# Kernel tuning notes

Measured on AMD Instinct MI355X. Metric: run time of the kernel, lower is better.

Reference implementation:

```python
import jax, jax.numpy as jnp
import numpy as np

N = 50000
E = 800000
IN_DIM = 128
HID = 64
OUT_DIM = 1
NEG_SLOPE = 0.2
EPS = 1e-16


def _glorot(key, shape):
    fan = shape[-1] + (shape[0] if len(shape) > 1 else shape[-1])
    lim = jnp.sqrt(6.0 / fan)
    return jax.random.uniform(key, shape, jnp.float32, -lim, lim)


def setup_inputs() -> dict:
    key = jax.random.key(0)
    ks = jax.random.split(key, 12)
    x = jax.random.normal(ks[0], (N, IN_DIM), jnp.float32)
    edge_index = jax.random.randint(ks[1], (2, E), 0, N, jnp.int64)
    # GATConv layer 1: in=128, out=64, heads=4, concat=True
    W1 = _glorot(ks[2], (4 * HID, IN_DIM))
    att_src1 = _glorot(ks[3], (4, HID))
    att_dst1 = _glorot(ks[4], (4, HID))
    b1 = jnp.zeros((4 * HID,), jnp.float32)
    # GATConv layer 2: in=256, out=64, heads=1, concat=True
    W2 = _glorot(ks[5], (HID, 4 * HID))
    att_src2 = _glorot(ks[6], (1, HID))
    att_dst2 = _glorot(ks[7], (1, HID))
    b2 = jnp.zeros((HID,), jnp.float32)
    # final Linear(hidden, 1)
    fc_w = _glorot(ks[8], (OUT_DIM, HID))
    fc_b = jnp.zeros((OUT_DIM,), jnp.float32)
    return {"x": x, "edge_index": edge_index, "W1": W1, "att_src1": att_src1,
            "att_dst1": att_dst1, "b1": b1, "W2": W2, "att_src2": att_src2,
            "att_dst2": att_dst2, "b2": b2, "fc_w": fc_w, "fc_b": fc_b}


def _gat_layer(x, src, dst, W, att_src, att_dst, bias, heads, out_ch):
    n = x.shape[0]
    xt = (x @ W.T).reshape(n, heads, out_ch)          # [N, H, C]
    a_src = jnp.sum(xt * att_src[None], axis=-1)      # [N, H]
    a_dst = jnp.sum(xt * att_dst[None], axis=-1)      # [N, H]
    e = a_src[src] + a_dst[dst]                       # [E', H]
    e = jnp.where(e > 0, e, NEG_SLOPE * e)            # LeakyReLU(0.2)
    # segment softmax over incoming edges of each dst node
    m = jax.ops.segment_max(e, dst, num_segments=n)
    e = jnp.exp(e - m[dst])
    s = jax.ops.segment_sum(e, dst, num_segments=n)
    alpha = e / (s[dst] + EPS)                        # [E', H]
    msg = xt[src] * alpha[:, :, None]                 # [E', H, C]
    out = jax.ops.segment_sum(msg, dst, num_segments=n)
    return out.reshape(n, heads * out_ch) + bias


def reference(x, edge_index, W1, att_src1, att_dst1, b1,
              W2, att_src2, att_dst2, b2, fc_w, fc_b):
    n = x.shape[0]
    # PyG GATConv default: add self-loops
    loops = jnp.arange(n, dtype=edge_index.dtype)
    src = jnp.concatenate([edge_index[0], loops])
    dst = jnp.concatenate([edge_index[1], loops])
    h = jax.nn.relu(_gat_layer(x, src, dst, W1, att_src1, att_dst1, b1, 4, HID))
    h = jax.nn.relu(_gat_layer(h, src, dst, W2, att_src2, att_dst2, b2, 1, HID))
    logits = h @ fc_w.T + fc_b                        # [N, 1]
    return jax.nn.sigmoid(logits).squeeze()
```

## Files before the change

### kernel.cpp

```cpp
#include <hip/hip_runtime.h>
#include <hip/hip_bf16.h>

#define NN 50000
#define EE 800000
#define ET (NN + EE)
#define SG ((NN + 255) / 256)

typedef __attribute__((ext_vector_type(8))) short short8;
typedef __attribute__((ext_vector_type(4))) float f32x4;

__device__ __forceinline__ float bf2f(unsigned short u) {
    union { unsigned int i; float f; } v; v.i = ((unsigned int)u) << 16; return v.f;
}
__device__ __forceinline__ unsigned short f2bf(float f) {
    __hip_bfloat16 h = __float2bfloat16(f);
    return *reinterpret_cast<unsigned short*>(&h);
}
__device__ __forceinline__ float lrelu(float e) { return e > 0.f ? e : 0.2f * e; }


__global__ void k_init_cnt(int* __restrict__ cnt) {
    int i = blockIdx.x * blockDim.x + threadIdx.x;
    if (i < NN) cnt[i] = 1;
}

__global__ void k_hist(const int* __restrict__ dst, int* __restrict__ cnt) {
    int i = blockIdx.x * blockDim.x + threadIdx.x;
    if (i < EE) atomicAdd(&cnt[dst[i]], 1);
}

__global__ __launch_bounds__(256) void k_scan1(const int* __restrict__ cnt,
                                               int* __restrict__ tmp, int* __restrict__ bsum) {
    int b = blockIdx.x, t = threadIdx.x, i = b * 256 + t;
    int lane = t & 63, w = t >> 6;
    int v = (i < NN) ? cnt[i] : 0;
    int s = v;
    #pragma unroll
    for (int off = 1; off < 64; off <<= 1) {
        int u = __shfl_up(s, off);
        if (lane >= off) s += u;
    }
    __shared__ int ws[4];
    if (lane == 63) ws[w] = s;
    __syncthreads();
    if (t == 0) {
        int a = 0;
        #pragma unroll
        for (int k = 0; k < 4; k++) { int x = ws[k]; ws[k] = a; a += x; }
        bsum[b] = a;
    }
    __syncthreads();
    s += ws[w];
    if (i < NN) tmp[i] = s;
}

__global__ __launch_bounds__(256) void k_scan2(const int* __restrict__ bsum, int* __restrict__ boff) {
    int t = threadIdx.x, lane = t & 63, w = t >> 6;
    int v = (t < SG) ? bsum[t] : 0;
    int s = v;
    #pragma unroll
    for (int off = 1; off < 64; off <<= 1) {
        int u = __shfl_up(s, off);
        if (lane >= off) s += u;
    }
    __shared__ int ws[4];
    if (lane == 63) ws[w] = s;
    __syncthreads();
    if (t == 0) {
        int a = 0;
        #pragma unroll
        for (int k = 0; k < 4; k++) { int x = ws[k]; ws[k] = a; a += x; }
    }
    __syncthreads();
    s += ws[w];
    if (t < SG) boff[t] = s - v;
}

__global__ void k_scan3_prep(const int* __restrict__ tmp, const int* __restrict__ boff,
                             int* __restrict__ rowptr, int* __restrict__ writeptr,
                             int* __restrict__ csr, int* __restrict__ dstarr) {
    int i = blockIdx.x * blockDim.x + threadIdx.x;
    if (i == 0) rowptr[0] = 0;
    if (i < NN) {
        int incl = tmp[i] + boff[i >> 8];
        rowptr[i + 1] = incl;
        int v = (i & 255) ? tmp[i - 1] + boff[i >> 8] : boff[i >> 8];
        csr[v] = i;
        dstarr[v] = i;
        writeptr[i] = v + 1;
    }
}

__global__ void k_scatter(const int* __restrict__ src, const int* __restrict__ dst,
                          int* __restrict__ writeptr, int* __restrict__ csr,
                          int* __restrict__ dstarr) {
    int i = blockIdx.x * blockDim.x + threadIdx.x;
    if (i < EE) {
        int d = dst[i];
        int pos = atomicAdd(&writeptr[d], 1);
        csr[pos] = src[i];
        dstarr[pos] = d;
    }
}

template<int K, int N, int NH, bool A_BF16>
__global__ __launch_bounds__(256) void k_gemm_mfma(
    const void* __restrict__ Aptr, const float* __restrict__ W,
    const float* __restrict__ atts, const float* __restrict__ attd,
    unsigned short* __restrict__ C, float* __restrict__ as_, float* __restrict__ ad_,
    int M)
{
    constexpr int KU  = K / 8;
    constexpr int KUH = KU / 2;
    constexpr int KC  = K / 32;
    constexpr int NW  = N / 4;
    constexpr int NI  = NW / 16;
    constexpr int ABYTES = 64 * KU * 16;
    constexpr int BBYTES = N * KUH * 16;
    constexpr int SMEM = ABYTES + BBYTES + (NH == 1 ? 2048 : 0);
    __shared__ char smem[SMEM];
    char* Ash = smem;
    char* Bsh = smem + ABYTES;
    unsigned short* Csh = (unsigned short*)smem;
    float* scsh = (float*)(smem + ABYTES + BBYTES);

    int t = threadIdx.x;
    int lane = t & 63, w = t >> 6;
    int colL = lane & 15, quad = lane >> 4;
    int m0 = blockIdx.x * 64;

    {
        constexpr int CNT = 64 * KU / 256;
        #pragma unroll
        for (int i = 0; i < CNT; i++) {
            int v = t + 256 * i;
            int m = v / KU, u = v % KU;
            int gr = m0 + m; if (gr >= M) gr = M - 1;
            short8 val;
            if (A_BF16) {
                val = *(const short8*)((const unsigned short*)Aptr + (size_t)gr * K + u * 8);
            } else {
                const float* Af = (const float*)Aptr;
                float4 lo = *(const float4*)(Af + (size_t)gr * K + u * 8);
                float4 hi = *(const float4*)(Af + (size_t)gr * K + u * 8 + 4);
                val[0] = (short)f2bf(lo.x); val[1] = (short)f2bf(lo.y);
                val[2] = (short)f2bf(lo.z); val[3] = (short)f2bf(lo.w);
                val[4] = (short)f2bf(hi.x); val[5] = (short)f2bf(hi.y);
                val[6] = (short)f2bf(hi.z); val[7] = (short)f2bf(hi.w);
            }
            *(short8*)(Ash + ((size_t)m * KU + (u ^ (m & 7))) * 16) = val;
        }
    }

    f32x4 acc[4][NI];
    #pragma unroll
    for (int mi = 0; mi < 4; mi++)
        #pragma unroll
        for (int ni = 0; ni < NI; ni++) acc[mi][ni] = (f32x4){0.f, 0.f, 0.f, 0.f};

    #pragma unroll
    for (int kh = 0; kh < 2; kh++) {
        __syncthreads();
        {
            constexpr int CNT = N * KUH / 256;
            #pragma unroll
            for (int i = 0; i < CNT; i++) {
                int v = t + 256 * i;
                int n = v / KUH, uu = v % KUH;
                int u = kh * KUH + uu;
                float4 lo = *(const float4*)(W + (size_t)n * K + u * 8);
                float4 hi = *(const float4*)(W + (size_t)n * K + u * 8 + 4);
                short8 val;
                val[0] = (short)f2bf(lo.x); val[1] = (short)f2bf(lo.y);
                val[2] = (short)f2bf(lo.z); val[3] = (short)f2bf(lo.w);
                val[4] = (short)f2bf(hi.x); val[5] = (short)f2bf(hi.y);
                val[6] = (short)f2bf(hi.z); val[7] = (short)f2bf(hi.w);
                *(short8*)(Bsh + ((size_t)n * KUH + (uu ^ (n & 7))) * 16) = val;
            }
        }
        __syncthreads();
        #pragma unroll
        for (int kcl = 0; kcl < KC / 2; kcl++) {
            int uA = (kh * (KC / 2) + kcl) * 4 + quad;
            int uB = kcl * 4 + quad;
            short8 bf[NI];
            #pragma unroll
            for (int ni = 0; ni < NI; ni++) {
                int n = w * NW + ni * 16 + colL;
                bf[ni] = *(const short8*)(Bsh + ((size_t)n * KUH + (uB ^ (n & 7))) * 16);
            }
            #pragma unroll
            for (int mi = 0; mi < 4; mi++) {
                int m = mi * 16 + colL;
                short8 af = *(const short8*)(Ash + ((size_t)m * KU + (uA ^ (m & 7))) * 16);
                #pragma unroll
                for (int ni = 0; ni < NI; ni++)
                    acc[mi][ni] = __builtin_amdgcn_mfma_f32_16x16x32_bf16(af, bf[ni], acc[mi][ni], 0, 0, 0);
            }
        }
    }
    __syncthreads();

    float asv[NI], adv[NI];
    #pragma unroll
    for (int ni = 0; ni < NI; ni++) {
        int na = (NH == 4) ? (w * 64 + ni * 16 + colL) : (w * 16 + colL);
        asv[ni] = atts[na];
        adv[ni] = attd[na];
    }
    #pragma unroll
    for (int mi = 0; mi < 4; mi++) {
        float ps[4] = {0.f, 0.f, 0.f, 0.f}, pd[4] = {0.f, 0.f, 0.f, 0.f};
        #pragma unroll
        for (int ni = 0; ni < NI; ni++)
            #pragma unroll
            for (int r = 0; r < 4; r++) {
                ps[r] += acc[mi][ni][r] * asv[ni];
                pd[r] += acc[mi][ni][r] * adv[ni];
            }
        #pragma unroll
        for (int off = 1; off < 16; off <<= 1)
            #pragma unroll
            for (int r = 0; r < 4; r++) {
                ps[r] += __shfl_xor(ps[r], off);
                pd[r] += __shfl_xor(pd[r], off);
            }
        if (colL == 0) {
            #pragma unroll
            for (int r = 0; r < 4; r++) {
                int rloc = mi * 16 + quad * 4 + r;
                if (NH == 4) {
                    int row = m0 + rloc;
                    if (row < M) {
                        as_[(size_t)row * 4 + w] = ps[r];
                        ad_[(size_t)row * 4 + w] = pd[r];
                    }
                } else {
                    scsh[(w * 64 + rloc) * 2 + 0] = ps[r];
                    scsh[(w * 64 + rloc) * 2 + 1] = pd[r];
                }
            }
        }
    }

    #pragma unroll
    for (int mi = 0; mi < 4; mi++)
        #pragma unroll
        for (int ni = 0; ni < NI; ni++)
            #pragma unroll
            for (int r = 0; r < 4; r++)
                Csh[(size_t)(mi * 16 + quad * 4 + r) * (N + 8) + w * NW + ni * 16 + colL] =
                    f2bf(acc[mi][ni][r]);
    __syncthreads();

    {
        constexpr int CNT = 64 * (N / 8) / 256;
        #pragma unroll
        for (int i = 0; i < CNT; i++) {
            int v = t + 256 * i;
            int m = v / (N / 8), u = v % (N / 8);
            int row = m0 + m;
            if (row < M)
                *(short8*)(C + (size_t)row * N + u * 8) =
                    *(const short8*)(Csh + (size_t)m * (N + 8) + u * 8);
        }
    }
    if (NH == 1 && t < 64) {
        int row = m0 + t;
        if (row < M) {
            float s = 0.f, d = 0.f;
            #pragma unroll
            for (int ww = 0; ww < 4; ww++) {
                s += scsh[(ww * 64 + t) * 2 + 0];
                d += scsh[(ww * 64 + t) * 2 + 1];
            }
            as_[row] = s;
            ad_[row] = d;
        }
    }
}

__global__ void k_escore1(const int* __restrict__ csr, const int* __restrict__ dstarr,
                          const float* __restrict__ as1, const float* __restrict__ ad1,
                          float* __restrict__ ew) {
    int i = blockIdx.x * blockDim.x + threadIdx.x;
    if (i < ET) {
        int s = csr[i], n = dstarr[i];
        float4 a = *(const float4*)(as1 + (size_t)s * 4);
        float4 d = *(const float4*)(ad1 + (size_t)n * 4);
        float4 e;
        e.x = __expf(lrelu(a.x + d.x));
        e.y = __expf(lrelu(a.y + d.y));
        e.z = __expf(lrelu(a.z + d.z));
        e.w = __expf(lrelu(a.w + d.w));
        *(float4*)(ew + (size_t)i * 4) = e;
    }
}

__global__ void k_escore2(const int* __restrict__ csr, const int* __restrict__ dstarr,
                          const float* __restrict__ as2, const float* __restrict__ ad2,
                          float* __restrict__ ew) {
    int i = blockIdx.x * blockDim.x + threadIdx.x;
    if (i < ET) {
        int s = csr[i], n = dstarr[i];
        ew[i] = __expf(lrelu(as2[s] + ad2[n]));
    }
}

__global__ __launch_bounds__(256) void k_l1_agg(
    const unsigned short* __restrict__ xt1, const float* __restrict__ ew,
    const int* __restrict__ rowptr, const int* __restrict__ csr,
    const float* __restrict__ b1, unsigned short* __restrict__ h1)
{
    int t = threadIdx.x;
    int lane = t & 63, w = t >> 6;
    int n = blockIdx.x * 4 + w;
    int beg = rowptr[n], deg = rowptr[n + 1] - beg;
    int half = lane >> 5, c = lane & 31, h = c >> 3;

    float acc[8] = {0.f, 0.f, 0.f, 0.f, 0.f, 0.f, 0.f, 0.f};
    float esum = 0.f;
    int j = 0;
    for (; j + 4 <= deg; j += 4) {
        int p = beg + j + half * 2;
        int s0 = csr[p], s1 = csr[p + 1];
        float e0 = ew[(size_t)p * 4 + h];
        float e1 = ew[(size_t)(p + 1) * 4 + h];
        short8 r0 = *(const short8*)(xt1 + (size_t)s0 * 256 + c * 8);
        short8 r1 = *(const short8*)(xt1 + (size_t)s1 * 256 + c * 8);
        esum += e0 + e1;
        #pragma unroll
        for (int k = 0; k < 8; k++)
            acc[k] += bf2f((unsigned short)r0[k]) * e0 + bf2f((unsigned short)r1[k]) * e1;
    }
    for (; j < deg; j += 2) {
        int jj = j + half;
        if (jj < deg) {
            int p = beg + jj;
            int s = csr[p];
            float e = ew[(size_t)p * 4 + h];
            short8 r = *(const short8*)(xt1 + (size_t)s * 256 + c * 8);
            esum += e;
            #pragma unroll
            for (int k = 0; k < 8; k++) acc[k] += bf2f((unsigned short)r[k]) * e;
        }
    }
    #pragma unroll
    for (int k = 0; k < 8; k++) acc[k] += __shfl_xor(acc[k], 32);
    esum += __shfl_xor(esum, 32);
    if (half == 0) {
        float rs = 1.f / (esum + 1e-16f);
        float4 bl = *(const float4*)(b1 + c * 8);
        float4 bh = *(const float4*)(b1 + c * 8 + 4);
        float bb[8] = {bl.x, bl.y, bl.z, bl.w, bh.x, bh.y, bh.z, bh.w};
        short8 o;
        #pragma unroll
        for (int k = 0; k < 8; k++)
            o[k] = (short)f2bf(fmaxf(acc[k] * rs + bb[k], 0.f));
        *(short8*)(h1 + (size_t)n * 256 + c * 8) = o;
    }
}

__global__ __launch_bounds__(256) void k_l2_agg(
    const unsigned short* __restrict__ xt2, const float* __restrict__ ew,
    const int* __restrict__ rowptr, const int* __restrict__ csr,
    const float* __restrict__ b2, const float* __restrict__ fcw, const float* __restrict__ fcb,
    float* __restrict__ out)
{
    int t = threadIdx.x;
    int lane = t & 63, w = t >> 6;
    int n = blockIdx.x * 4 + w;
    int beg = rowptr[n], deg = rowptr[n + 1] - beg;
    int half = lane >> 5, c = lane & 31;

    float a0 = 0.f, a1 = 0.f, esum = 0.f;
    int j = 0;
    for (; j + 4 <= deg; j += 4) {
        int p = beg + j + half * 2;
        int s0 = csr[p], s1 = csr[p + 1];
        float e0 = ew[p], e1 = ew[p + 1];
        unsigned int r0 = *(const unsigned int*)(xt2 + (size_t)s0 * 64 + c * 2);
        unsigned int r1 = *(const unsigned int*)(xt2 + (size_t)s1 * 64 + c * 2);
        esum += e0 + e1;
        a0 += bf2f(r0 & 0xffff) * e0 + bf2f(r1 & 0xffff) * e1;
        a1 += bf2f(r0 >> 16) * e0 + bf2f(r1 >> 16) * e1;
    }
    for (; j < deg; j += 2) {
        int jj = j + half;
        if (jj < deg) {
            int p = beg + jj;
            int s = csr[p];
            float e = ew[p];
            unsigned int r = *(const unsigned int*)(xt2 + (size_t)s * 64 + c * 2);
            esum += e;
            a0 += bf2f(r & 0xffff) * e;
            a1 += bf2f(r >> 16) * e;
        }
    }
    a0 += __shfl_xor(a0, 32);
    a1 += __shfl_xor(a1, 32);
    esum += __shfl_xor(esum, 32);
    if (half == 0) {
        float rs = 1.f / (esum + 1e-16f);
        float o0 = fmaxf(a0 * rs + b2[c * 2], 0.f);
        float o1 = fmaxf(a1 * rs + b2[c * 2 + 1], 0.f);
        float z = o0 * fcw[c * 2] + o1 * fcw[c * 2 + 1];
        #pragma unroll
        for (int off = 16; off; off >>= 1) z += __shfl_xor(z, off);
        if (c == 0) out[n] = 1.f / (1.f + __expf(-(z + fcb[0])));
    }
}


extern "C" void kernel_launch(void* const* d_in, const int* in_sizes, int n_in,
                              void* d_out, int out_size, void* d_ws, size_t ws_size,
                              hipStream_t stream) {
    const float* x    = (const float*)d_in[0];
    const int*   ei   = (const int*)d_in[1];
    const float* W1   = (const float*)d_in[2];
    const float* as1w = (const float*)d_in[3];
    const float* ad1w = (const float*)d_in[4];
    const float* b1   = (const float*)d_in[5];
    const float* W2   = (const float*)d_in[6];
    const float* as2w = (const float*)d_in[7];
    const float* ad2w = (const float*)d_in[8];
    const float* b2   = (const float*)d_in[9];
    const float* fcw  = (const float*)d_in[10];
    const float* fcb  = (const float*)d_in[11];
    float* out = (float*)d_out;

    const int* src = ei;
    const int* dst = ei + EE;

    char* base = (char*)d_ws;
    size_t off = 0;
    auto alloc = [&](size_t bytes) -> void* {
        void* p = base + off;
        off = (off + bytes + 255) & ~(size_t)255;
        return p;
    };
    int*   rowptr   = (int*)alloc((NN + 1) * sizeof(int));
    int*   cnt      = (int*)alloc(NN * sizeof(int));
    int*   tmp      = (int*)alloc(NN * sizeof(int));
    int*   bsum     = (int*)alloc(SG * sizeof(int));
    int*   boff     = (int*)alloc(SG * sizeof(int));
    int*   writeptr = (int*)alloc(NN * sizeof(int));
    int*   csr      = (int*)alloc(ET * sizeof(int));
    int*   dstarr   = (int*)alloc(ET * sizeof(int));
    float* ew1      = (float*)alloc((size_t)ET * 4 * sizeof(float));
    unsigned short* xt1 = (unsigned short*)alloc((size_t)NN * 256 * sizeof(unsigned short));
    unsigned short* h1  = (unsigned short*)alloc((size_t)NN * 256 * sizeof(unsigned short));
    float* as1      = (float*)alloc(NN * 4 * sizeof(float));
    float* ad1      = (float*)alloc(NN * 4 * sizeof(float));
    float* as2      = (float*)alloc(NN * sizeof(float));
    float* ad2      = (float*)alloc(NN * sizeof(float));
    unsigned short* xt2 = xt1;
    float* ew2      = ew1;

    k_init_cnt<<<(NN + 255) / 256, 256, 0, stream>>>(cnt);
    k_hist<<<(EE + 255) / 256, 256, 0, stream>>>(dst, cnt);
    k_scan1<<<SG, 256, 0, stream>>>(cnt, tmp, bsum);
    k_scan2<<<1, 256, 0, stream>>>(bsum, boff);
    k_scan3_prep<<<SG, 256, 0, stream>>>(tmp, boff, rowptr, writeptr, csr, dstarr);
    k_scatter<<<(EE + 255) / 256, 256, 0, stream>>>(src, dst, writeptr, csr, dstarr);

    int gblocks = (NN + 63) / 64;
    k_gemm_mfma<128, 256, 4, false><<<gblocks, 256, 0, stream>>>(
        x, W1, as1w, ad1w, xt1, as1, ad1, NN);
    k_escore1<<<(ET + 255) / 256, 256, 0, stream>>>(csr, dstarr, as1, ad1, ew1);
    k_l1_agg<<<(NN + 3) / 4, 256, 0, stream>>>(xt1, ew1, rowptr, csr, b1, h1);
    k_gemm_mfma<256, 64, 1, true><<<gblocks, 256, 0, stream>>>(
        h1, W2, as2w, ad2w, xt2, as2, ad2, NN);
    k_escore2<<<(ET + 255) / 256, 256, 0, stream>>>(csr, dstarr, as2, ad2, ew2);
    k_l2_agg<<<(NN + 3) / 4, 256, 0, stream>>>(xt2, ew2, rowptr, csr, b2, fcw, fcb, out);
}
```

Measured before the change: 329.3 us.

## Drop dstarr, compute edge scores per node, and unroll aggregation loops to 4 edges

Removes the per-edge destination array, so the scatter and prep kernels no longer write it. The edge-score kernels become thread-per-node loops over each CSR row, reusing the destination score instead of reading it per edge. The aggregation kernels now process four edges per half-wave per iteration, putting more gathers in flight. The cost is that the per-node score loops are uncoalesced and unbalanced across threads: each thread walks its own row with strided accesses, and only about 196 blocks are launched.

```diff
diff --git a/kernel.cpp b/kernel.cpp
--- a/kernel.cpp
+++ b/kernel.cpp
@@ -78,7 +78,7 @@
 
 __global__ void k_scan3_prep(const int* __restrict__ tmp, const int* __restrict__ boff,
                              int* __restrict__ rowptr, int* __restrict__ writeptr,
-                             int* __restrict__ csr, int* __restrict__ dstarr) {
+                             int* __restrict__ csr) {
     int i = blockIdx.x * blockDim.x + threadIdx.x;
     if (i == 0) rowptr[0] = 0;
     if (i < NN) {
@@ -86,20 +86,16 @@
         rowptr[i + 1] = incl;
         int v = (i & 255) ? tmp[i - 1] + boff[i >> 8] : boff[i >> 8];
         csr[v] = i;
-        dstarr[v] = i;
         writeptr[i] = v + 1;
     }
 }
 
 __global__ void k_scatter(const int* __restrict__ src, const int* __restrict__ dst,
-                          int* __restrict__ writeptr, int* __restrict__ csr,
-                          int* __restrict__ dstarr) {
+                          int* __restrict__ writeptr, int* __restrict__ csr) {
     int i = blockIdx.x * blockDim.x + threadIdx.x;
     if (i < EE) {
-        int d = dst[i];
-        int pos = atomicAdd(&writeptr[d], 1);
+        int pos = atomicAdd(&writeptr[dst[i]], 1);
         csr[pos] = src[i];
-        dstarr[pos] = d;
     }
 }
 
@@ -280,30 +276,37 @@
     }
 }
 
-__global__ void k_escore1(const int* __restrict__ csr, const int* __restrict__ dstarr,
+__global__ void k_escore1(const int* __restrict__ rowptr, const int* __restrict__ csr,
                           const float* __restrict__ as1, const float* __restrict__ ad1,
                           float* __restrict__ ew) {
-    int i = blockIdx.x * blockDim.x + threadIdx.x;
-    if (i < ET) {
-        int s = csr[i], n = dstarr[i];
-        float4 a = *(const float4*)(as1 + (size_t)s * 4);
+    int n = blockIdx.x * blockDim.x + threadIdx.x;
+    if (n < NN) {
+        int beg = rowptr[n], end = rowptr[n + 1];
         float4 d = *(const float4*)(ad1 + (size_t)n * 4);
-        float4 e;
-        e.x = __expf(lrelu(a.x + d.x));
-        e.y = __expf(lrelu(a.y + d.y));
-        e.z = __expf(lrelu(a.z + d.z));
-        e.w = __expf(lrelu(a.w + d.w));
-        *(float4*)(ew + (size_t)i * 4) = e;
-    }
-}
-
-__global__ void k_escore2(const int* __restrict__ csr, const int* __restrict__ dstarr,
+        for (int p = beg; p < end; p++) {
+            int s = csr[p];
+            float4 a = *(const float4*)(as1 + (size_t)s * 4);
+            float4 e;
+            e.x = __expf(lrelu(a.x + d.x));
+            e.y = __expf(lrelu(a.y + d.y));
+            e.z = __expf(lrelu(a.z + d.z));
+            e.w = __expf(lrelu(a.w + d.w));
+            *(float4*)(ew + (size_t)p * 4) = e;
+        }
+    }
+}
+
+__global__ void k_escore2(const int* __restrict__ rowptr, const int* __restrict__ csr,
                           const float* __restrict__ as2, const float* __restrict__ ad2,
                           float* __restrict__ ew) {
-    int i = blockIdx.x * blockDim.x + threadIdx.x;
-    if (i < ET) {
-        int s = csr[i], n = dstarr[i];
-        ew[i] = __expf(lrelu(as2[s] + ad2[n]));
+    int n = blockIdx.x * blockDim.x + threadIdx.x;
+    if (n < NN) {
+        int beg = rowptr[n], end = rowptr[n + 1];
+        float d = ad2[n];
+        for (int p = beg; p < end; p++) {
+            int s = csr[p];
+            ew[p] = __expf(lrelu(as2[s] + d));
+        }
     }
 }
 
@@ -321,17 +324,22 @@
     float acc[8] = {0.f, 0.f, 0.f, 0.f, 0.f, 0.f, 0.f, 0.f};
     float esum = 0.f;
     int j = 0;
-    for (; j + 4 <= deg; j += 4) {
-        int p = beg + j + half * 2;
-        int s0 = csr[p], s1 = csr[p + 1];
+    for (; j + 8 <= deg; j += 8) {
+        int p = beg + j + half * 4;
+        int s0 = csr[p], s1 = csr[p + 1], s2 = csr[p + 2], s3 = csr[p + 3];
         float e0 = ew[(size_t)p * 4 + h];
         float e1 = ew[(size_t)(p + 1) * 4 + h];
+        float e2 = ew[(size_t)(p + 2) * 4 + h];
+        float e3 = ew[(size_t)(p + 3) * 4 + h];
         short8 r0 = *(const short8*)(xt1 + (size_t)s0 * 256 + c * 8);
         short8 r1 = *(const short8*)(xt1 + (size_t)s1 * 256 + c * 8);
-        esum += e0 + e1;
+        short8 r2 = *(const short8*)(xt1 + (size_t)s2 * 256 + c * 8);
+        short8 r3 = *(const short8*)(xt1 + (size_t)s3 * 256 + c * 8);
+        esum += (e0 + e1) + (e2 + e3);
         #pragma unroll
         for (int k = 0; k < 8; k++)
-            acc[k] += bf2f((unsigned short)r0[k]) * e0 + bf2f((unsigned short)r1[k]) * e1;
+            acc[k] += bf2f((unsigned short)r0[k]) * e0 + bf2f((unsigned short)r1[k]) * e1
+                    + bf2f((unsigned short)r2[k]) * e2 + bf2f((unsigned short)r3[k]) * e3;
     }
     for (; j < deg; j += 2) {
         int jj = j + half;
@@ -375,15 +383,19 @@
 
     float a0 = 0.f, a1 = 0.f, esum = 0.f;
     int j = 0;
-    for (; j + 4 <= deg; j += 4) {
-        int p = beg + j + half * 2;
-        int s0 = csr[p], s1 = csr[p + 1];
-        float e0 = ew[p], e1 = ew[p + 1];
+    for (; j + 8 <= deg; j += 8) {
+        int p = beg + j + half * 4;
+        int s0 = csr[p], s1 = csr[p + 1], s2 = csr[p + 2], s3 = csr[p + 3];
+        float e0 = ew[p], e1 = ew[p + 1], e2 = ew[p + 2], e3 = ew[p + 3];
         unsigned int r0 = *(const unsigned int*)(xt2 + (size_t)s0 * 64 + c * 2);
         unsigned int r1 = *(const unsigned int*)(xt2 + (size_t)s1 * 64 + c * 2);
-        esum += e0 + e1;
-        a0 += bf2f(r0 & 0xffff) * e0 + bf2f(r1 & 0xffff) * e1;
-        a1 += bf2f(r0 >> 16) * e0 + bf2f(r1 >> 16) * e1;
+        unsigned int r2 = *(const unsigned int*)(xt2 + (size_t)s2 * 64 + c * 2);
+        unsigned int r3 = *(const unsigned int*)(xt2 + (size_t)s3 * 64 + c * 2);
+        esum += (e0 + e1) + (e2 + e3);
+        a0 += bf2f(r0 & 0xffff) * e0 + bf2f(r1 & 0xffff) * e1
+            + bf2f(r2 & 0xffff) * e2 + bf2f(r3 & 0xffff) * e3;
+        a1 += bf2f(r0 >> 16) * e0 + bf2f(r1 >> 16) * e1
+            + bf2f(r2 >> 16) * e2 + bf2f(r3 >> 16) * e3;
     }
     for (; j < deg; j += 2) {
         int jj = j + half;
@@ -446,7 +458,6 @@
     int*   boff     = (int*)alloc(SG * sizeof(int));
     int*   writeptr = (int*)alloc(NN * sizeof(int));
     int*   csr      = (int*)alloc(ET * sizeof(int));
-    int*   dstarr   = (int*)alloc(ET * sizeof(int));
     float* ew1      = (float*)alloc((size_t)ET * 4 * sizeof(float));
     unsigned short* xt1 = (unsigned short*)alloc((size_t)NN * 256 * sizeof(unsigned short));
     unsigned short* h1  = (unsigned short*)alloc((size_t)NN * 256 * sizeof(unsigned short));
@@ -461,16 +472,16 @@
     k_hist<<<(EE + 255) / 256, 256, 0, stream>>>(dst, cnt);
     k_scan1<<<SG, 256, 0, stream>>>(cnt, tmp, bsum);
     k_scan2<<<1, 256, 0, stream>>>(bsum, boff);
-    k_scan3_prep<<<SG, 256, 0, stream>>>(tmp, boff, rowptr, writeptr, csr, dstarr);
-    k_scatter<<<(EE + 255) / 256, 256, 0, stream>>>(src, dst, writeptr, csr, dstarr);
+    k_scan3_prep<<<SG, 256, 0, stream>>>(tmp, boff, rowptr, writeptr, csr);
+    k_scatter<<<(EE + 255) / 256, 256, 0, stream>>>(src, dst, writeptr, csr);
 
     int gblocks = (NN + 63) / 64;
     k_gemm_mfma<128, 256, 4, false><<<gblocks, 256, 0, stream>>>(
         x, W1, as1w, ad1w, xt1, as1, ad1, NN);
-    k_escore1<<<(ET + 255) / 256, 256, 0, stream>>>(csr, dstarr, as1, ad1, ew1);
+    k_escore1<<<(NN + 255) / 256, 256, 0, stream>>>(rowptr, csr, as1, ad1, ew1);
     k_l1_agg<<<(NN + 3) / 4, 256, 0, stream>>>(xt1, ew1, rowptr, csr, b1, h1);
     k_gemm_mfma<256, 64, 1, true><<<gblocks, 256, 0, stream>>>(
         h1, W2, as2w, ad2w, xt2, as2, ad2, NN);
-    k_escore2<<<(ET + 255) / 256, 256, 0, stream>>>(csr, dstarr, as2, ad2, ew2);
+    k_escore2<<<(NN + 255) / 256, 256, 0, stream>>>(rowptr, csr, as2, ad2, ew2);
     k_l2_agg<<<(NN + 3) / 4, 256, 0, stream>>>(xt2, ew2, rowptr, csr, b2, fcw, fcb, out);
 }
```

After: 339.6 us. 1.03x slower.

## Slice layer-1 aggregation by feature columns and store edge weights head-major

Applied to the files above, without the earlier changes.

Edge weights for layer 1 are now stored head-major (one contiguous array per head). Layer-1 aggregation is split into 8 column slices per group of 16 nodes, and each wave handles 8 edges at a time with 4 columns per lane. This is meant to make each block's gathers touch a narrow slice of xt1, which may improve cache locality when blocks with the same slice run together. Layer-2 aggregation is also unrolled to 4 edges per half-wave to raise memory-level parallelism. The trade-off is that csr and rowptr are re-read once per slice, and the loop runs padded lanes on the last partial group of edges.

```diff
diff --git a/kernel.cpp b/kernel.cpp
--- a/kernel.cpp
+++ b/kernel.cpp
@@ -282,18 +282,16 @@
 
 __global__ void k_escore1(const int* __restrict__ csr, const int* __restrict__ dstarr,
                           const float* __restrict__ as1, const float* __restrict__ ad1,
-                          float* __restrict__ ew) {
+                          float* __restrict__ ewT) {
     int i = blockIdx.x * blockDim.x + threadIdx.x;
     if (i < ET) {
         int s = csr[i], n = dstarr[i];
         float4 a = *(const float4*)(as1 + (size_t)s * 4);
         float4 d = *(const float4*)(ad1 + (size_t)n * 4);
-        float4 e;
-        e.x = __expf(lrelu(a.x + d.x));
-        e.y = __expf(lrelu(a.y + d.y));
-        e.z = __expf(lrelu(a.z + d.z));
-        e.w = __expf(lrelu(a.w + d.w));
-        *(float4*)(ew + (size_t)i * 4) = e;
+        ewT[0 * (size_t)ET + i] = __expf(lrelu(a.x + d.x));
+        ewT[1 * (size_t)ET + i] = __expf(lrelu(a.y + d.y));
+        ewT[2 * (size_t)ET + i] = __expf(lrelu(a.z + d.z));
+        ewT[3 * (size_t)ET + i] = __expf(lrelu(a.w + d.w));
     }
 }
 
@@ -308,56 +306,56 @@
 }
 
 __global__ __launch_bounds__(256) void k_l1_agg(
-    const unsigned short* __restrict__ xt1, const float* __restrict__ ew,
+    const unsigned short* __restrict__ xt1, const float* __restrict__ ewT,
     const int* __restrict__ rowptr, const int* __restrict__ csr,
     const float* __restrict__ b1, unsigned short* __restrict__ h1)
 {
     int t = threadIdx.x;
     int lane = t & 63, w = t >> 6;
-    int n = blockIdx.x * 4 + w;
-    int beg = rowptr[n], deg = rowptr[n + 1] - beg;
-    int half = lane >> 5, c = lane & 31, h = c >> 3;
-
-    float acc[8] = {0.f, 0.f, 0.f, 0.f, 0.f, 0.f, 0.f, 0.f};
-    float esum = 0.f;
-    int j = 0;
-    for (; j + 4 <= deg; j += 4) {
-        int p = beg + j + half * 2;
-        int s0 = csr[p], s1 = csr[p + 1];
-        float e0 = ew[(size_t)p * 4 + h];
-        float e1 = ew[(size_t)(p + 1) * 4 + h];
-        short8 r0 = *(const short8*)(xt1 + (size_t)s0 * 256 + c * 8);
-        short8 r1 = *(const short8*)(xt1 + (size_t)s1 * 256 + c * 8);
-        esum += e0 + e1;
-        #pragma unroll
-        for (int k = 0; k < 8; k++)
-            acc[k] += bf2f((unsigned short)r0[k]) * e0 + bf2f((unsigned short)r1[k]) * e1;
-    }
-    for (; j < deg; j += 2) {
-        int jj = j + half;
-        if (jj < deg) {
-            int p = beg + jj;
-            int s = csr[p];
-            float e = ew[(size_t)p * 4 + h];
-            short8 r = *(const short8*)(xt1 + (size_t)s * 256 + c * 8);
+    int slice = blockIdx.x & 7;
+    int nb = blockIdx.x >> 3;
+    int c0 = slice * 32;
+    const float* ewp = ewT + (size_t)(slice >> 1) * ET;
+    int q = lane >> 3;
+    int cl = lane & 7;
+
+    float4 bv = *(const float4*)(b1 + c0 + cl * 4);
+
+    #pragma unroll
+    for (int rep = 0; rep < 4; rep++) {
+        int n = nb * 16 + w + rep * 4;
+        int beg = rowptr[n], end = rowptr[n + 1];
+        float a0 = 0.f, a1 = 0.f, a2 = 0.f, a3 = 0.f, esum = 0.f;
+        for (int p0 = beg; p0 < end; p0 += 8) {
+            int p = p0 + q;
+            int pc = min(p, end - 1);
+            int s = csr[pc];
+            float e = ewp[pc];
+            if (p >= end) e = 0.f;
+            ushort4 r = *(const ushort4*)(xt1 + (size_t)s * 256 + c0 + cl * 4);
             esum += e;
-            #pragma unroll
-            for (int k = 0; k < 8; k++) acc[k] += bf2f((unsigned short)r[k]) * e;
-        }
-    }
-    #pragma unroll
-    for (int k = 0; k < 8; k++) acc[k] += __shfl_xor(acc[k], 32);
-    esum += __shfl_xor(esum, 32);
-    if (half == 0) {
-        float rs = 1.f / (esum + 1e-16f);
-        float4 bl = *(const float4*)(b1 + c * 8);
-        float4 bh = *(const float4*)(b1 + c * 8 + 4);
-        float bb[8] = {bl.x, bl.y, bl.z, bl.w, bh.x, bh.y, bh.z, bh.w};
-        short8 o;
-        #pragma unroll
-        for (int k = 0; k < 8; k++)
-            o[k] = (short)f2bf(fmaxf(acc[k] * rs + bb[k], 0.f));
-        *(short8*)(h1 + (size_t)n * 256 + c * 8) = o;
+            a0 += bf2f(r.x) * e;
+            a1 += bf2f(r.y) * e;
+            a2 += bf2f(r.z) * e;
+            a3 += bf2f(r.w) * e;
+        }
+        #pragma unroll
+        for (int off = 8; off < 64; off <<= 1) {
+            a0 += __shfl_xor(a0, off);
+            a1 += __shfl_xor(a1, off);
+            a2 += __shfl_xor(a2, off);
+            a3 += __shfl_xor(a3, off);
+            esum += __shfl_xor(esum, off);
+        }
+        if (q == 0) {
+            float rs = 1.f / (esum + 1e-16f);
+            ushort4 o;
+            o.x = f2bf(fmaxf(a0 * rs + bv.x, 0.f));
+            o.y = f2bf(fmaxf(a1 * rs + bv.y, 0.f));
+            o.z = f2bf(fmaxf(a2 * rs + bv.z, 0.f));
+            o.w = f2bf(fmaxf(a3 * rs + bv.w, 0.f));
+            *(ushort4*)(h1 + (size_t)n * 256 + c0 + cl * 4) = o;
+        }
     }
 }
 
@@ -375,15 +373,19 @@
 
     float a0 = 0.f, a1 = 0.f, esum = 0.f;
     int j = 0;
-    for (; j + 4 <= deg; j += 4) {
-        int p = beg + j + half * 2;
-        int s0 = csr[p], s1 = csr[p + 1];
-        float e0 = ew[p], e1 = ew[p + 1];
+    for (; j + 8 <= deg; j += 8) {
+        int p = beg + j + half * 4;
+        int s0 = csr[p], s1 = csr[p + 1], s2 = csr[p + 2], s3 = csr[p + 3];
+        float e0 = ew[p], e1 = ew[p + 1], e2 = ew[p + 2], e3 = ew[p + 3];
         unsigned int r0 = *(const unsigned int*)(xt2 + (size_t)s0 * 64 + c * 2);
         unsigned int r1 = *(const unsigned int*)(xt2 + (size_t)s1 * 64 + c * 2);
-        esum += e0 + e1;
-        a0 += bf2f(r0 & 0xffff) * e0 + bf2f(r1 & 0xffff) * e1;
-        a1 += bf2f(r0 >> 16) * e0 + bf2f(r1 >> 16) * e1;
+        unsigned int r2 = *(const unsigned int*)(xt2 + (size_t)s2 * 64 + c * 2);
+        unsigned int r3 = *(const unsigned int*)(xt2 + (size_t)s3 * 64 + c * 2);
+        esum += (e0 + e1) + (e2 + e3);
+        a0 += bf2f(r0 & 0xffff) * e0 + bf2f(r1 & 0xffff) * e1
+            + bf2f(r2 & 0xffff) * e2 + bf2f(r3 & 0xffff) * e3;
+        a1 += bf2f(r0 >> 16) * e0 + bf2f(r1 >> 16) * e1
+            + bf2f(r2 >> 16) * e2 + bf2f(r3 >> 16) * e3;
     }
     for (; j < deg; j += 2) {
         int jj = j + half;
@@ -447,7 +449,7 @@
     int*   writeptr = (int*)alloc(NN * sizeof(int));
     int*   csr      = (int*)alloc(ET * sizeof(int));
     int*   dstarr   = (int*)alloc(ET * sizeof(int));
-    float* ew1      = (float*)alloc((size_t)ET * 4 * sizeof(float));
+    float* ewT      = (float*)alloc((size_t)ET * 4 * sizeof(float));
     unsigned short* xt1 = (unsigned short*)alloc((size_t)NN * 256 * sizeof(unsigned short));
     unsigned short* h1  = (unsigned short*)alloc((size_t)NN * 256 * sizeof(unsigned short));
     float* as1      = (float*)alloc(NN * 4 * sizeof(float));
@@ -455,7 +457,7 @@
     float* as2      = (float*)alloc(NN * sizeof(float));
     float* ad2      = (float*)alloc(NN * sizeof(float));
     unsigned short* xt2 = xt1;
-    float* ew2      = ew1;
+    float* ew2      = ewT;
 
     k_init_cnt<<<(NN + 255) / 256, 256, 0, stream>>>(cnt);
     k_hist<<<(EE + 255) / 256, 256, 0, stream>>>(dst, cnt);
@@ -467,8 +469,8 @@
     int gblocks = (NN + 63) / 64;
     k_gemm_mfma<128, 256, 4, false><<<gblocks, 256, 0, stream>>>(
         x, W1, as1w, ad1w, xt1, as1, ad1, NN);
-    k_escore1<<<(ET + 255) / 256, 256, 0, stream>>>(csr, dstarr, as1, ad1, ew1);
-    k_l1_agg<<<(NN + 3) / 4, 256, 0, stream>>>(xt1, ew1, rowptr, csr, b1, h1);
+    k_escore1<<<(ET + 255) / 256, 256, 0, stream>>>(csr, dstarr, as1, ad1, ewT);
+    k_l1_agg<<<8 * (NN / 16), 256, 0, stream>>>(xt1, ewT, rowptr, csr, b1, h1);
     k_gemm_mfma<256, 64, 1, true><<<gblocks, 256, 0, stream>>>(
         h1, W2, as2w, ad2w, xt2, as2, ad2, NN);
     k_escore2<<<(ET + 255) / 256, 256, 0, stream>>>(csr, dstarr, as2, ad2, ew2);
```

New measurement: 392.7 us. 19.3% more time.

## Fuse edge-score computation into aggregation and co-schedule scatter with layer-1 GEMM

Applied to the files above, without the earlier changes.

Drops the separate edge-score kernels and the per-edge score buffers. Each aggregation now recomputes exp(lrelu(a_src+a_dst)) inline from per-node attention values. The dstarr array goes away, and the self-loop counts are folded into the scan by adding the index instead of running a count-init kernel. The CSR scatter is interleaved with the layer-1 GEMM in one launch, using block-id partitioning so scatter blocks run alongside GEMM blocks. This removes several launches and a large amount of edge-array memory traffic, at the cost of extra gathers and exp calls inside the aggregation loops.

```diff
diff --git a/kernel.cpp b/kernel.cpp
--- a/kernel.cpp
+++ b/kernel.cpp
@@ -5,6 +5,7 @@
 #define EE 800000
 #define ET (NN + EE)
 #define SG ((NN + 255) / 256)
+#define GB1 ((NN + 63) / 64)
 
 typedef __attribute__((ext_vector_type(8))) short short8;
 typedef __attribute__((ext_vector_type(4))) float f32x4;
@@ -18,11 +19,6 @@
 }
 __device__ __forceinline__ float lrelu(float e) { return e > 0.f ? e : 0.2f * e; }
 
-
-__global__ void k_init_cnt(int* __restrict__ cnt) {
-    int i = blockIdx.x * blockDim.x + threadIdx.x;
-    if (i < NN) cnt[i] = 1;
-}
 
 __global__ void k_hist(const int* __restrict__ dst, int* __restrict__ cnt) {
     int i = blockIdx.x * blockDim.x + threadIdx.x;
@@ -78,34 +74,22 @@
 
 __global__ void k_scan3_prep(const int* __restrict__ tmp, const int* __restrict__ boff,
                              int* __restrict__ rowptr, int* __restrict__ writeptr,
-                             int* __restrict__ csr, int* __restrict__ dstarr) {
+                             int* __restrict__ csr) {
     int i = blockIdx.x * blockDim.x + threadIdx.x;
     if (i == 0) rowptr[0] = 0;
     if (i < NN) {
-        int incl = tmp[i] + boff[i >> 8];
+        int base = boff[i >> 8];
+        int incl = tmp[i] + base + i + 1;
         rowptr[i + 1] = incl;
-        int v = (i & 255) ? tmp[i - 1] + boff[i >> 8] : boff[i >> 8];
-        csr[v] = i;
-        dstarr[v] = i;
-        writeptr[i] = v + 1;
-    }
-}
-
-__global__ void k_scatter(const int* __restrict__ src, const int* __restrict__ dst,
-                          int* __restrict__ writeptr, int* __restrict__ csr,
-                          int* __restrict__ dstarr) {
-    int i = blockIdx.x * blockDim.x + threadIdx.x;
-    if (i < EE) {
-        int d = dst[i];
-        int pos = atomicAdd(&writeptr[d], 1);
-        csr[pos] = src[i];
-        dstarr[pos] = d;
+        int excl = ((i & 255) ? tmp[i - 1] + base : base) + i;
+        csr[excl] = i;
+        writeptr[i] = excl + 1;
     }
 }
 
 template<int K, int N, int NH, bool A_BF16>
-__global__ __launch_bounds__(256) void k_gemm_mfma(
-    const void* __restrict__ Aptr, const float* __restrict__ W,
+__device__ __forceinline__ void gemm_body(
+    int bid, const void* __restrict__ Aptr, const float* __restrict__ W,
     const float* __restrict__ atts, const float* __restrict__ attd,
     unsigned short* __restrict__ C, float* __restrict__ as_, float* __restrict__ ad_,
     int M)
@@ -127,7 +111,7 @@
     int t = threadIdx.x;
     int lane = t & 63, w = t >> 6;
     int colL = lane & 15, quad = lane >> 4;
-    int m0 = blockIdx.x * 64;
+    int m0 = bid * 64;
 
     {
         constexpr int CNT = 64 * KU / 256;
@@ -280,43 +264,52 @@
     }
 }
 
-__global__ void k_escore1(const int* __restrict__ csr, const int* __restrict__ dstarr,
-                          const float* __restrict__ as1, const float* __restrict__ ad1,
-                          float* __restrict__ ew) {
-    int i = blockIdx.x * blockDim.x + threadIdx.x;
-    if (i < ET) {
-        int s = csr[i], n = dstarr[i];
-        float4 a = *(const float4*)(as1 + (size_t)s * 4);
-        float4 d = *(const float4*)(ad1 + (size_t)n * 4);
-        float4 e;
-        e.x = __expf(lrelu(a.x + d.x));
-        e.y = __expf(lrelu(a.y + d.y));
-        e.z = __expf(lrelu(a.z + d.z));
-        e.w = __expf(lrelu(a.w + d.w));
-        *(float4*)(ew + (size_t)i * 4) = e;
-    }
-}
-
-__global__ void k_escore2(const int* __restrict__ csr, const int* __restrict__ dstarr,
-                          const float* __restrict__ as2, const float* __restrict__ ad2,
-                          float* __restrict__ ew) {
-    int i = blockIdx.x * blockDim.x + threadIdx.x;
-    if (i < ET) {
-        int s = csr[i], n = dstarr[i];
-        ew[i] = __expf(lrelu(as2[s] + ad2[n]));
+template<int K, int N, int NH, bool A_BF16>
+__global__ __launch_bounds__(256) void k_gemm_mfma(
+    const void* __restrict__ Aptr, const float* __restrict__ W,
+    const float* __restrict__ atts, const float* __restrict__ attd,
+    unsigned short* __restrict__ C, float* __restrict__ as_, float* __restrict__ ad_,
+    int M)
+{
+    gemm_body<K, N, NH, A_BF16>(blockIdx.x, Aptr, W, atts, attd, C, as_, ad_, M);
+}
+
+__global__ __launch_bounds__(256) void k_gemm1_scatter(
+    const void* __restrict__ Aptr, const float* __restrict__ W,
+    const float* __restrict__ atts, const float* __restrict__ attd,
+    unsigned short* __restrict__ C, float* __restrict__ as_, float* __restrict__ ad_,
+    int M,
+    const int* __restrict__ src, const int* __restrict__ dst,
+    int* __restrict__ writeptr, int* __restrict__ csr)
+{
+    int bid = blockIdx.x;
+    int g = bid / 5, r = bid % 5;
+    if (r == 0 && g < GB1) {
+        gemm_body<128, 256, 4, false>(g, Aptr, W, atts, attd, C, as_, ad_, M);
+    } else {
+        int ng = (r == 0) ? g : g + 1;
+        if (ng > GB1) ng = GB1;
+        int sb = bid - ng;
+        int i = sb * 256 + threadIdx.x;
+        if (i < EE) {
+            int pos = atomicAdd(&writeptr[dst[i]], 1);
+            csr[pos] = src[i];
+        }
     }
 }
 
 __global__ __launch_bounds__(256) void k_l1_agg(
-    const unsigned short* __restrict__ xt1, const float* __restrict__ ew,
-    const int* __restrict__ rowptr, const int* __restrict__ csr,
-    const float* __restrict__ b1, unsigned short* __restrict__ h1)
+    const unsigned short* __restrict__ xt1, const float* __restrict__ as1,
+    const float* __restrict__ ad1, const int* __restrict__ rowptr,
+    const int* __restrict__ csr, const float* __restrict__ b1,
+    unsigned short* __restrict__ h1)
 {
     int t = threadIdx.x;
     int lane = t & 63, w = t >> 6;
     int n = blockIdx.x * 4 + w;
     int beg = rowptr[n], deg = rowptr[n + 1] - beg;
     int half = lane >> 5, c = lane & 31, h = c >> 3;
+    float adh = ad1[n * 4 + h];
 
     float acc[8] = {0.f, 0.f, 0.f, 0.f, 0.f, 0.f, 0.f, 0.f};
     float esum = 0.f;
@@ -324,8 +317,8 @@
     for (; j + 4 <= deg; j += 4) {
         int p = beg + j + half * 2;
         int s0 = csr[p], s1 = csr[p + 1];
-        float e0 = ew[(size_t)p * 4 + h];
-        float e1 = ew[(size_t)(p + 1) * 4 + h];
+        float e0 = __expf(lrelu(as1[s0 * 4 + h] + adh));
+        float e1 = __expf(lrelu(as1[s1 * 4 + h] + adh));
         short8 r0 = *(const short8*)(xt1 + (size_t)s0 * 256 + c * 8);
         short8 r1 = *(const short8*)(xt1 + (size_t)s1 * 256 + c * 8);
         esum += e0 + e1;
@@ -338,7 +331,7 @@
         if (jj < deg) {
             int p = beg + jj;
             int s = csr[p];
-            float e = ew[(size_t)p * 4 + h];
+            float e = __expf(lrelu(as1[s * 4 + h] + adh));
             short8 r = *(const short8*)(xt1 + (size_t)s * 256 + c * 8);
             esum += e;
             #pragma unroll
@@ -362,9 +355,10 @@
 }
 
 __global__ __launch_bounds__(256) void k_l2_agg(
-    const unsigned short* __restrict__ xt2, const float* __restrict__ ew,
-    const int* __restrict__ rowptr, const int* __restrict__ csr,
-    const float* __restrict__ b2, const float* __restrict__ fcw, const float* __restrict__ fcb,
+    const unsigned short* __restrict__ xt2, const float* __restrict__ as2,
+    const float* __restrict__ ad2, const int* __restrict__ rowptr,
+    const int* __restrict__ csr, const float* __restrict__ b2,
+    const float* __restrict__ fcw, const float* __restrict__ fcb,
     float* __restrict__ out)
 {
     int t = threadIdx.x;
@@ -372,13 +366,15 @@
     int n = blockIdx.x * 4 + w;
     int beg = rowptr[n], deg = rowptr[n + 1] - beg;
     int half = lane >> 5, c = lane & 31;
+    float adv = ad2[n];
 
     float a0 = 0.f, a1 = 0.f, esum = 0.f;
     int j = 0;
     for (; j + 4 <= deg; j += 4) {
         int p = beg + j + half * 2;
         int s0 = csr[p], s1 = csr[p + 1];
-        float e0 = ew[p], e1 = ew[p + 1];
+        float e0 = __expf(lrelu(as2[s0] + adv));
+        float e1 = __expf(lrelu(as2[s1] + adv));
         unsigned int r0 = *(const unsigned int*)(xt2 + (size_t)s0 * 64 + c * 2);
         unsigned int r1 = *(const unsigned int*)(xt2 + (size_t)s1 * 64 + c * 2);
         esum += e0 + e1;
@@ -390,7 +386,7 @@
         if (jj < deg) {
             int p = beg + jj;
             int s = csr[p];
-            float e = ew[p];
+            float e = __expf(lrelu(as2[s] + adv));
             unsigned int r = *(const unsigned int*)(xt2 + (size_t)s * 64 + c * 2);
             esum += e;
             a0 += bf2f(r & 0xffff) * e;
@@ -446,8 +442,6 @@
     int*   boff     = (int*)alloc(SG * sizeof(int));
     int*   writeptr = (int*)alloc(NN * sizeof(int));
     int*   csr      = (int*)alloc(ET * sizeof(int));
-    int*   dstarr   = (int*)alloc(ET * sizeof(int));
-    float* ew1      = (float*)alloc((size_t)ET * 4 * sizeof(float));
     unsigned short* xt1 = (unsigned short*)alloc((size_t)NN * 256 * sizeof(unsigned short));
     unsigned short* h1  = (unsigned short*)alloc((size_t)NN * 256 * sizeof(unsigned short));
     float* as1      = (float*)alloc(NN * 4 * sizeof(float));
@@ -455,22 +449,19 @@
     float* as2      = (float*)alloc(NN * sizeof(float));
     float* ad2      = (float*)alloc(NN * sizeof(float));
     unsigned short* xt2 = xt1;
-    float* ew2      = ew1;
-
-    k_init_cnt<<<(NN + 255) / 256, 256, 0, stream>>>(cnt);
+
+    hipMemsetAsync(cnt, 0, NN * sizeof(int), stream);
     k_hist<<<(EE + 255) / 256, 256, 0, stream>>>(dst, cnt);
     k_scan1<<<SG, 256, 0, stream>>>(cnt, tmp, bsum);
     k_scan2<<<1, 256, 0, stream>>>(bsum, boff);
-    k_scan3_prep<<<SG, 256, 0, stream>>>(tmp, boff, rowptr, writeptr, csr, dstarr);
-    k_scatter<<<(EE + 255) / 256, 256, 0, stream>>>(src, dst, writeptr, csr, dstarr);
-
-    int gblocks = (NN + 63) / 64;
-    k_gemm_mfma<128, 256, 4, false><<<gblocks, 256, 0, stream>>>(
-        x, W1, as1w, ad1w, xt1, as1, ad1, NN);
-    k_escore1<<<(ET + 255) / 256, 256, 0, stream>>>(csr, dstarr, as1, ad1, ew1);
-    k_l1_agg<<<(NN + 3) / 4, 256, 0, stream>>>(xt1, ew1, rowptr, csr, b1, h1);
-    k_gemm_mfma<256, 64, 1, true><<<gblocks, 256, 0, stream>>>(
+    k_scan3_prep<<<SG, 256, 0, stream>>>(tmp, boff, rowptr, writeptr, csr);
+
+    int fused_blocks = GB1 + (EE + 255) / 256;
+    k_gemm1_scatter<<<fused_blocks, 256, 0, stream>>>(
+        x, W1, as1w, ad1w, xt1, as1, ad1, NN, src, dst, writeptr, csr);
+
+    k_l1_agg<<<(NN + 3) / 4, 256, 0, stream>>>(xt1, as1, ad1, rowptr, csr, b1, h1);
+    k_gemm_mfma<256, 64, 1, true><<<GB1, 256, 0, stream>>>(
         h1, W2, as2w, ad2w, xt2, as2, ad2, NN);
-    k_escore2<<<(ET + 255) / 256, 256, 0, stream>>>(csr, dstarr, as2, ad2, ew2);
-    k_l2_agg<<<(NN + 3) / 4, 256, 0, stream>>>(xt2, ew2, rowptr, csr, b2, fcw, fcb, out);
-}
+    k_l2_agg<<<(NN + 3) / 4, 256, 0, stream>>>(xt2, as2, ad2, rowptr, csr, b2, fcw, fcb, out);
+}
```

Result: faster. 289.9 us (-12.0%).
